# Optimization experiments

Hardware: AMD Instinct MI355X
Metric: run time of the kernel (lower is better)

## Reference

```python
import jax, jax.numpy as jnp
import numpy as np

B, N, M, D = 8, 1024, 2048, 1024


def setup_inputs() -> dict:
    key = jax.random.key(0)
    k1, k2, k3 = jax.random.split(key, 3)
    text_features = jax.random.normal(k1, (B, N, D), dtype=jnp.float32)
    audio_features = jax.random.normal(k2, (B, M, D), dtype=jnp.float32)
    sigma = jnp.ones((1,), dtype=jnp.float32)  # learnable bandwidth, initial_sigma=1.0
    # audio lengths in [M//4, M) so no softmax row is fully masked
    audio_lengths = jnp.maximum(
        jax.random.randint(k3, (B,), 0, M), M // 4
    ).astype(jnp.int32)
    return {
        "text_features": text_features,
        "audio_features": audio_features,
        "sigma": sigma,
        "audio_lengths": audio_lengths,
    }


def reference(text_features, audio_features, sigma, audio_lengths):
    b, n, d = text_features.shape
    m = audio_features.shape[1]
    s = jnp.abs(sigma[0]) + 1e-8

    # QK^T / sqrt(d)  -> (B, N, M)
    scores = jnp.einsum("bnd,bmd->bnm", text_features, audio_features) / jnp.sqrt(
        jnp.float32(d)
    )

    # Gaussian relative positional bias: -|i/N - j/M|^2 / (2 sigma^2)
    text_pos = jnp.arange(n, dtype=jnp.float32) / n    # (N,)
    audio_pos = jnp.arange(m, dtype=jnp.float32) / m   # (M,)
    d_rel = jnp.abs(text_pos[:, None] - audio_pos[None, :])  # (N, M)
    scores = scores - d_rel**2 / (2.0 * s * s)

    # mask padded audio positions per batch element
    valid = jnp.arange(m)[None, :] < audio_lengths[:, None]  # (B, M) bool
    scores = jnp.where(valid[:, None, :], scores, -jnp.inf)

    attention_weights = jax.nn.softmax(scores, axis=-1)  # (B, N, M)
    enhanced = jnp.einsum("bnm,bmd->bnd", attention_weights, audio_features)
    return enhanced, attention_weights
```

## Files before the change

### kernel.cpp

```cpp
#include <hip/hip_runtime.h>
#include <hip/hip_bf16.h>

#define BB 8
#define NN 1024
#define MM 2048
#define DD 1024

typedef __attribute__((ext_vector_type(8))) __bf16 bfrag8;
typedef __attribute__((ext_vector_type(4))) float ffrag4;

__device__ __forceinline__ unsigned short f2bf(float f) {
  union { float f; unsigned u; } x; x.f = f;
  unsigned r = x.u + 0x7FFFu + ((x.u >> 16) & 1u);
  return (unsigned short)(r >> 16);
}

__device__ __forceinline__ void gload_lds16(const unsigned short* g, unsigned short* l) {
  __builtin_amdgcn_global_load_lds(
      (const __attribute__((address_space(1))) void*)g,
      (__attribute__((address_space(3))) void*)l, 16, 0, 0);
}

#define SCHED0() __builtin_amdgcn_sched_barrier(0)
#define MFMA16x16x32 __builtin_amdgcn_mfma_f32_16x16x32_bf16

__device__ __forceinline__ void stage_half(const unsigned short* gbase, int ldk,
                                           unsigned short* ldst,
                                           int w, int r0, int slog) {
  const unsigned short* g = gbase + (size_t)(w * 8 + r0) * ldk + slog;
  gload_lds16(g, ldst + w * 512);
  gload_lds16(g + (size_t)64 * ldk, ldst + 4096 + w * 512);
}

__device__ __forceinline__ void stage_op32(const unsigned short* gbase, int ldk,
                                           unsigned short* L,
                                           int w, int srow, int sloc) {
  const unsigned short* g0 = gbase + (size_t)(w * 32 + srow) * ldk + sloc;
  gload_lds16(g0, L + w * 1024);
  gload_lds16(g0 + (size_t)16 * ldk, L + w * 1024 + 512);
}

#define TSTR 68
__global__ __launch_bounds__(256) void ta_prep(
    const float* __restrict__ Q, const float* __restrict__ V,
    unsigned short* __restrict__ Qbf,
    unsigned short* __restrict__ Kbf, unsigned short* __restrict__ VT,
    float* __restrict__ sums)
{
  __shared__ unsigned short Tls[64 * TSTR];
  const int bid = blockIdx.x;
  const int t = threadIdx.x;

  if (bid < 4096) {
    int tt = bid * 256 + t;
    const float4* src = reinterpret_cast<const float4*>(Q) + tt * 2;
    float4 a = src[0], b = src[1];
    ushort4 lo = { f2bf(a.x), f2bf(a.y), f2bf(a.z), f2bf(a.w) };
    ushort4 hi = { f2bf(b.x), f2bf(b.y), f2bf(b.z), f2bf(b.w) };
    ushort4* dst = reinterpret_cast<ushort4*>(Qbf) + tt * 2;
    dst[0] = lo; dst[1] = hi;
  } else if (bid < 8192) {
    const int id = bid - 4096;
    const int dt = id & 15;
    const int mt = (id >> 4) & 31;
    const int b  = id >> 9;

    const float* Vb = V + (size_t)b * MM * DD + (size_t)(mt * 64) * DD + dt * 64;
#pragma unroll
    for (int it = 0; it < 4; ++it) {
      int slot = t + 256 * it;
      int row  = slot >> 4;
      int c4   = slot & 15;
      float4 a = *reinterpret_cast<const float4*>(Vb + (size_t)row * DD + c4 * 4);
      ushort4 h = { f2bf(a.x), f2bf(a.y), f2bf(a.z), f2bf(a.w) };
      *reinterpret_cast<ushort4*>(&Tls[row * TSTR + c4 * 4]) = h;
    }
    __syncthreads();

    unsigned short* Kb = Kbf + (size_t)b * MM * DD + (size_t)(mt * 64) * DD + dt * 64;
    unsigned short* Vt = VT  + (size_t)b * DD * MM + (size_t)(dt * 64) * MM + mt * 64;
#pragma unroll
    for (int it = 0; it < 4; ++it) {
      int slot = t + 256 * it;
      int row  = slot >> 4;
      int c4   = slot & 15;
      *reinterpret_cast<ushort4*>(Kb + (size_t)row * DD + c4 * 4) =
          *reinterpret_cast<const ushort4*>(&Tls[row * TSTR + c4 * 4]);
      ushort4 tv = { Tls[(c4 * 4 + 0) * TSTR + row],
                     Tls[(c4 * 4 + 1) * TSTR + row],
                     Tls[(c4 * 4 + 2) * TSTR + row],
                     Tls[(c4 * 4 + 3) * TSTR + row] };
      *reinterpret_cast<ushort4*>(Vt + (size_t)row * MM + c4 * 4) = tv;
    }
  } else {
    int tt = (bid - 8192) * 256 + t;
    sums[tt] = 0.0f;
  }
}

__global__ void ta_zero(float* __restrict__ sums) {
  int t = blockIdx.x * 256 + threadIdx.x;
  if (t < BB * NN) sums[t] = 0.0f;
}

__global__ __launch_bounds__(512, 2) void ta_gemm1x(
    const unsigned short* __restrict__ Q,
    const unsigned short* __restrict__ K,
    const float* __restrict__ sigma,
    const int* __restrict__ lens,
    unsigned short* __restrict__ Ebf,
    float* __restrict__ rowsum)
{
  const int lin = blockIdx.x + 8 * (blockIdx.y + 4 * blockIdx.z);
  const int wid = (lin & 7) * 32 + (lin >> 3);
  const int bj = wid & 7, bi = (wid >> 3) & 3, b = wid >> 5;

  const int t = threadIdx.x;
  const int lane = t & 63, w = t >> 6;
  const int wr = w >> 2, wc = w & 3;
  __shared__ unsigned short S[73728];

  const unsigned short* Qb = Q + (size_t)b * NN * DD + (size_t)(bi * 256) * DD;
  const unsigned short* Kb = K + (size_t)b * MM * DD + (size_t)(bj * 256) * DD;

  const int r  = lane & 15, qd = lane >> 4;
  const int srow = lane >> 2;
  const int sloc = ((lane & 3) ^ (srow & 3)) << 3;
  const int fco  = (qd ^ (r & 3)) << 3;

  ffrag4 acc[8][4] = {};

  {
    stage_op32(Qb,      DD, &S[0],            w, srow, sloc);
    stage_op32(Kb,      DD, &S[8192],         w, srow, sloc);
    stage_op32(Qb + 32, DD, &S[16384],        w, srow, sloc);
    stage_op32(Kb + 32, DD, &S[16384 + 8192], w, srow, sloc);
    stage_op32(Qb + 64, DD, &S[32768],        w, srow, sloc);
    stage_op32(Kb + 64, DD, &S[32768 + 8192], w, srow, sloc);
    asm volatile("s_waitcnt vmcnt(8)" ::: "memory");
    __builtin_amdgcn_s_barrier();
  }

#pragma unroll 4
  for (int kt = 0; kt < 32; ++kt) {
    unsigned short* Buf = &S[(kt & 3) * 16384];

    if (kt + 3 < 32) {
      unsigned short* D = &S[((kt + 3) & 3) * 16384];
      const int k0 = (kt + 3) * 32;
      stage_op32(Qb + k0, DD, D,        w, srow, sloc);
      stage_op32(Kb + k0, DD, D + 8192, w, srow, sloc);
    }

    bfrag8 af[8], bf[4];
    const unsigned short* Ar = Buf + (wr * 128 + r) * 32 + fco;
    const unsigned short* Br = Buf + 8192 + (wc * 64 + r) * 32 + fco;
#pragma unroll
    for (int mi = 0; mi < 8; ++mi)
      af[mi] = *reinterpret_cast<const bfrag8*>(Ar + mi * 512);
#pragma unroll
    for (int nj = 0; nj < 4; ++nj)
      bf[nj] = *reinterpret_cast<const bfrag8*>(Br + nj * 512);

    asm volatile("s_waitcnt lgkmcnt(0)" ::: "memory");
    SCHED0(); __builtin_amdgcn_s_setprio(1);
#pragma unroll
    for (int mi = 0; mi < 8; ++mi)
#pragma unroll
      for (int nj = 0; nj < 4; ++nj)
        acc[mi][nj] = MFMA16x16x32(af[mi], bf[nj], acc[mi][nj], 0, 0, 0);
    __builtin_amdgcn_s_setprio(0); SCHED0();

    if (kt < 29)       { asm volatile("s_waitcnt vmcnt(8)" ::: "memory"); }
    else if (kt == 29) { asm volatile("s_waitcnt vmcnt(4)" ::: "memory"); }
    else if (kt == 30) { asm volatile("s_waitcnt vmcnt(0)" ::: "memory"); }
    if (kt < 31) __builtin_amdgcn_s_barrier();
  }
  __syncthreads();

  const float sg = fabsf(sigma[0]) + 1e-8f;
  const float inv2s2 = 1.0f / (2.0f * sg * sg);
  const int len = lens[b];
  unsigned short* Erow = Ebf + (size_t)b * NN * MM;
  float* sums = rowsum + (size_t)b * NN;
  const int ibase = bi * 256 + wr * 128;
  const int jbase = bj * 256 + wc * 64;
  unsigned short* W = &S[w * 9216];

#pragma unroll
  for (int mi = 0; mi < 8; ++mi) {
#pragma unroll
    for (int v = 0; v < 4; ++v) {
      int lrow = mi * 16 + qd * 4 + v;
      int i = ibase + lrow;
      float psum = 0.0f;
#pragma unroll
      for (int nj = 0; nj < 4; ++nj) {
        int j = jbase + nj * 16 + r;
        float e = 0.0f;
        if (j < len) {
          float dr = (float)i * (1.0f / (float)NN) - (float)j * (1.0f / (float)MM);
          float sc = acc[mi][nj][v] * 0.03125f - dr * dr * inv2s2;
          e = __expf(fminf(sc, 30.0f));
        }
        psum += e;
        W[lrow * 72 + nj * 16 + r] = f2bf(e);
      }
      psum += __shfl_xor(psum, 1);
      psum += __shfl_xor(psum, 2);
      psum += __shfl_xor(psum, 4);
      psum += __shfl_xor(psum, 8);
      if (r == 0) atomicAdd(&sums[i], psum);
    }
  }
  asm volatile("s_waitcnt lgkmcnt(0)" ::: "memory");
  const int rrow = lane >> 3, c8 = lane & 7;
#pragma unroll
  for (int pp = 0; pp < 16; ++pp) {
    int row = pp * 8 + rrow;
    uint4 val = *reinterpret_cast<const uint4*>(&W[row * 72 + c8 * 8]);
    *reinterpret_cast<uint4*>(Erow + (size_t)(ibase + row) * MM + jbase + c8 * 8) = val;
  }
}

__global__ __launch_bounds__(512, 2) void ta_gemm2x(
    const unsigned short* __restrict__ E,
    const unsigned short* __restrict__ VT,
    const float* __restrict__ rowsum,
    float* __restrict__ O,
    float* __restrict__ attn)
{
  const int lin = blockIdx.x + 4 * (blockIdx.y + 8 * blockIdx.z);
  const int wid = (lin & 7) * 32 + (lin >> 3);
  const int bd = wid & 3, bi = (wid >> 2) & 7, b = wid >> 5;

  const int t = threadIdx.x;
  const int lane = t & 63, w = t >> 6;
  const int wr = w >> 2, wc = w & 3;
  __shared__ unsigned short S[73728];

  const unsigned short* Eb = E  + (size_t)b * NN * MM + (size_t)(bi * 128) * MM;
  const unsigned short* Vb = VT + (size_t)b * DD * MM + (size_t)(bd * 256) * MM;

  const int r  = lane & 15, qd = lane >> 4;
  const int r0 = (lane >> 3) & 7;
  const int slog = ((lane & 7) ^ r0) << 3;
  const int cs0 = ((qd)     ^ (r & 7)) << 3;
  const int cs1 = ((4 + qd) ^ (r & 7)) << 3;

  ffrag4 acc[4][4] = {};

  const float* rsB = rowsum + (size_t)b * NN;
  const int arow = t >> 2;
  const int lcb  = (t & 3) * 2;
  const int apc0 = (lcb)     ^ (arow & 7);
  const int apc1 = (lcb + 1) ^ (arow & 7);
  const float ainv = 1.0f / fmaxf(rsB[bi * 128 + arow], 1e-30f);
  float* attnRowBase = attn + ((size_t)b * NN + bi * 128 + arow) * MM;

  {
    stage_half(Eb,                        MM, &S[0],     w, r0, slog);
    stage_half(Vb,                        MM, &S[8192],  w, r0, slog);
    stage_half(Vb + (size_t)128 * MM,     MM, &S[16384], w, r0, slog);
    stage_half(Eb + 64,                    MM, &S[24576],         w, r0, slog);
    stage_half(Vb + 64,                    MM, &S[24576 + 8192],  w, r0, slog);
    stage_half(Vb + (size_t)128 * MM + 64, MM, &S[24576 + 16384], w, r0, slog);
    asm volatile("s_waitcnt vmcnt(6)" ::: "memory");
    __builtin_amdgcn_s_barrier();
  }

  int cur = 0;
  for (int kt = 0; kt < 32; ++kt) {
    unsigned short* Tb = &S[cur * 24576];
    unsigned short* Ab = Tb;
    unsigned short* Bb = Tb + 8192 + (wc >> 1) * 8192;
    const int arb = wr * 64;
    const int brb = (wc & 1) * 64;

    if (kt + 2 < 32) {
      int nb = cur + 2; if (nb >= 3) nb -= 3;
      unsigned short* D = &S[nb * 24576];
      const int k0 = (kt + 2) * 64;
      stage_half(Eb + k0,                    MM, D,         w, r0, slog);
      stage_half(Vb + k0,                    MM, D + 8192,  w, r0, slog);
      stage_half(Vb + (size_t)128 * MM + k0, MM, D + 16384, w, r0, slog);
    }

    bfrag8 af[4][2], bf[4][2];
#pragma unroll
    for (int mi = 0; mi < 4; ++mi) {
      const unsigned short* a = &Ab[(arb + mi * 16 + r) * 64];
      af[mi][0] = *reinterpret_cast<const bfrag8*>(a + cs0);
      af[mi][1] = *reinterpret_cast<const bfrag8*>(a + cs1);
    }
#pragma unroll
    for (int nj = 0; nj < 4; ++nj) {
      const unsigned short* bp = &Bb[(brb + nj * 16 + r) * 64];
      bf[nj][0] = *reinterpret_cast<const bfrag8*>(bp + cs0);
      bf[nj][1] = *reinterpret_cast<const bfrag8*>(bp + cs1);
    }

    if ((kt >> 3) == bd) {
      uint4 av0 = *reinterpret_cast<const uint4*>(&Ab[arow * 64 + apc0 * 8]);
      uint4 av1 = *reinterpret_cast<const uint4*>(&Ab[arow * 64 + apc1 * 8]);
      float* dst = attnRowBase + kt * 64 + lcb * 8;
      unsigned u[8] = { av0.x, av0.y, av0.z, av0.w, av1.x, av1.y, av1.z, av1.w };
      float o[16];
#pragma unroll
      for (int k2 = 0; k2 < 8; ++k2) {
        union { unsigned u; float f; } lo, hi;
        lo.u = u[k2] << 16; hi.u = u[k2] & 0xFFFF0000u;
        o[2 * k2]     = lo.f * ainv;
        o[2 * k2 + 1] = hi.f * ainv;
      }
      float4* d4 = reinterpret_cast<float4*>(dst);
      float4 f0 = { o[0],  o[1],  o[2],  o[3]  };
      float4 f1 = { o[4],  o[5],  o[6],  o[7]  };
      float4 f2 = { o[8],  o[9],  o[10], o[11] };
      float4 f3 = { o[12], o[13], o[14], o[15] };
      d4[0] = f0; d4[1] = f1; d4[2] = f2; d4[3] = f3;
    }

    asm volatile("s_waitcnt lgkmcnt(0)" ::: "memory");
    SCHED0(); __builtin_amdgcn_s_setprio(1);
#pragma unroll
    for (int mi = 0; mi < 4; ++mi)
#pragma unroll
      for (int nj = 0; nj < 4; ++nj) {
        acc[mi][nj] = MFMA16x16x32(af[mi][0], bf[nj][0], acc[mi][nj], 0, 0, 0);
        acc[mi][nj] = MFMA16x16x32(af[mi][1], bf[nj][1], acc[mi][nj], 0, 0, 0);
      }
    __builtin_amdgcn_s_setprio(0); SCHED0();

    if (kt < 30)       { asm volatile("s_waitcnt vmcnt(6)" ::: "memory"); }
    else if (kt == 30) { asm volatile("s_waitcnt vmcnt(0)" ::: "memory"); }
    if (kt < 31) __builtin_amdgcn_s_barrier();
    cur += 1; if (cur == 3) cur = 0;
  }

  float* Ob = O + (size_t)b * NN * DD;
  const int ibase = bi * 128 + wr * 64;
  const int dbase = bd * 256 + wc * 64;
#pragma unroll
  for (int mi = 0; mi < 4; ++mi) {
#pragma unroll
    for (int v = 0; v < 4; ++v) {
      int i = ibase + mi * 16 + qd * 4 + v;
      float inv = 1.0f / fmaxf(rsB[i], 1e-30f);
#pragma unroll
      for (int nj = 0; nj < 4; ++nj) {
        int d = dbase + nj * 16 + r;
        Ob[(size_t)i * DD + d] = acc[mi][nj][v] * inv;
      }
    }
  }
}

#define LDA 40
__global__ __launch_bounds__(256) void tb_gemm1e(
    const float* __restrict__ Q, const float* __restrict__ K,
    const float* __restrict__ sigma, const int* __restrict__ lens,
    float* __restrict__ attn, float* __restrict__ rowsum)
{
  const int bj = blockIdx.x, bi = blockIdx.y, b = blockIdx.z;
  const int t = threadIdx.x;
  const int lane = t & 63;
  const int w = t >> 6;
  const int wi = w >> 1, wj = w & 1;
  __shared__ unsigned short Als[128 * LDA];
  __shared__ unsigned short Bls[128 * LDA];
  const float* Qb = Q + (size_t)b * NN * DD + (size_t)(bi * 128) * DD;
  const float* Kb = K + (size_t)b * MM * DD + (size_t)(bj * 128) * DD;
  ffrag4 acc[4][4] = {};
  const int r = lane & 15;
  const int koff = (lane >> 4) * 8;
  for (int k0 = 0; k0 < DD; k0 += 32) {
#pragma unroll
    for (int it = 0; it < 4; ++it) {
      int slot = t + 256 * it;
      int row = slot >> 3, c4 = slot & 7;
      float4 qa = *reinterpret_cast<const float4*>(Qb + (size_t)row * DD + k0 + c4 * 4);
      float4 ka = *reinterpret_cast<const float4*>(Kb + (size_t)row * DD + k0 + c4 * 4);
      ushort4 qh = { f2bf(qa.x), f2bf(qa.y), f2bf(qa.z), f2bf(qa.w) };
      ushort4 kh = { f2bf(ka.x), f2bf(ka.y), f2bf(ka.z), f2bf(ka.w) };
      *reinterpret_cast<ushort4*>(&Als[row * LDA + c4 * 4]) = qh;
      *reinterpret_cast<ushort4*>(&Bls[row * LDA + c4 * 4]) = kh;
    }
    __syncthreads();
    bfrag8 af[4], bf[4];
#pragma unroll
    for (int ti = 0; ti < 4; ++ti)
      af[ti] = *reinterpret_cast<const bfrag8*>(&Als[(wi * 64 + ti * 16 + r) * LDA + koff]);
#pragma unroll
    for (int tj = 0; tj < 4; ++tj)
      bf[tj] = *reinterpret_cast<const bfrag8*>(&Bls[(wj * 64 + tj * 16 + r) * LDA + koff]);
#pragma unroll
    for (int ti = 0; ti < 4; ++ti)
#pragma unroll
      for (int tj = 0; tj < 4; ++tj)
        acc[ti][tj] = MFMA16x16x32(af[ti], bf[tj], acc[ti][tj], 0, 0, 0);
    __syncthreads();
  }
  const float s = fabsf(sigma[0]) + 1e-8f;
  const float inv2s2 = 1.0f / (2.0f * s * s);
  const int len = lens[b];
  float* Prow = attn + (size_t)b * NN * MM;
  float* sums = rowsum + (size_t)b * NN;
  const int ibase = bi * 128 + wi * 64;
  const int jbase = bj * 128 + wj * 64;
  const int quad = lane >> 4;
#pragma unroll
  for (int ti = 0; ti < 4; ++ti) {
#pragma unroll
    for (int v = 0; v < 4; ++v) {
      int i = ibase + ti * 16 + quad * 4 + v;
      float psum = 0.0f;
#pragma unroll
      for (int tj = 0; tj < 4; ++tj) {
        int j = jbase + tj * 16 + r;
        float e = 0.0f;
        if (j < len) {
          float dr = (float)i * (1.0f / (float)NN) - (float)j * (1.0f / (float)MM);
          float sc = acc[ti][tj][v] * 0.03125f - dr * dr * inv2s2;
          e = __expf(fminf(sc, 30.0f));
        }
        psum += e;
        Prow[(size_t)i * MM + j] = e;
      }
      psum += __shfl_xor(psum, 1);
      psum += __shfl_xor(psum, 2);
      psum += __shfl_xor(psum, 4);
      psum += __shfl_xor(psum, 8);
      if (r == 0) atomicAdd(&sums[i], psum);
    }
  }
}

__global__ __launch_bounds__(256) void tb_norm(float* __restrict__ attn,
                                               const float* __restrict__ sums) {
  int t = blockIdx.x * 256 + threadIdx.x;
  int row = t >> 9;
  const float inv = 1.0f / fmaxf(sums[row], 1e-30f);
  float4* p = reinterpret_cast<float4*>(attn) + t;
  float4 x = *p;
  x.x *= inv; x.y *= inv; x.z *= inv; x.w *= inv;
  *p = x;
}

__global__ __launch_bounds__(256) void tb_gemm2(
    const float* __restrict__ P, const float* __restrict__ V, float* __restrict__ O)
{
  const int bd = blockIdx.x, bi = blockIdx.y, b = blockIdx.z;
  const int t = threadIdx.x;
  const int lane = t & 63;
  const int w = t >> 6;
  const int wi = w >> 1, wj = w & 1;
  __shared__ unsigned short Pls[128 * LDA];
  __shared__ unsigned short Vls[128 * LDA];
  const float* Pb = P + (size_t)b * NN * MM + (size_t)(bi * 128) * MM;
  const float* Vb = V + (size_t)b * MM * DD + bd * 128;
  ffrag4 acc[4][4] = {};
  const int r = lane & 15;
  const int koff = (lane >> 4) * 8;
  const int vd = t & 127;
  const int vmb = (t >> 7) * 16;
  for (int k0 = 0; k0 < MM; k0 += 32) {
#pragma unroll
    for (int it = 0; it < 4; ++it) {
      int slot = t + 256 * it;
      int row = slot >> 3, c4 = slot & 7;
      float4 pa = *reinterpret_cast<const float4*>(Pb + (size_t)row * MM + k0 + c4 * 4);
      ushort4 ph = { f2bf(pa.x), f2bf(pa.y), f2bf(pa.z), f2bf(pa.w) };
      *reinterpret_cast<ushort4*>(&Pls[row * LDA + c4 * 4]) = ph;
    }
    union { unsigned short h[16]; uint4 q[2]; } hv;
#pragma unroll
    for (int i = 0; i < 16; ++i)
      hv.h[i] = f2bf(Vb[(size_t)(k0 + vmb + i) * DD + vd]);
    *reinterpret_cast<uint4*>(&Vls[vd * LDA + vmb]) = hv.q[0];
    *reinterpret_cast<uint4*>(&Vls[vd * LDA + vmb + 8]) = hv.q[1];
    __syncthreads();
    bfrag8 af[4], bf[4];
#pragma unroll
    for (int ti = 0; ti < 4; ++ti)
      af[ti] = *reinterpret_cast<const bfrag8*>(&Pls[(wi * 64 + ti * 16 + r) * LDA + koff]);
#pragma unroll
    for (int tj = 0; tj < 4; ++tj)
      bf[tj] = *reinterpret_cast<const bfrag8*>(&Vls[(wj * 64 + tj * 16 + r) * LDA + koff]);
#pragma unroll
    for (int ti = 0; ti < 4; ++ti)
#pragma unroll
      for (int tj = 0; tj < 4; ++tj)
        acc[ti][tj] = MFMA16x16x32(af[ti], bf[tj], acc[ti][tj], 0, 0, 0);
    __syncthreads();
  }
  float* Ob = O + (size_t)b * NN * DD;
  const int ibase = bi * 128 + wi * 64;
  const int dbase = bd * 128 + wj * 64;
#pragma unroll
  for (int ti = 0; ti < 4; ++ti) {
#pragma unroll
    for (int tj = 0; tj < 4; ++tj) {
      int d = dbase + tj * 16 + r;
#pragma unroll
      for (int v = 0; v < 4; ++v) {
        int i = ibase + ti * 16 + (lane >> 4) * 4 + v;
        Ob[(size_t)i * DD + d] = acc[ti][tj][v];
      }
    }
  }
}

extern "C" void kernel_launch(void* const* d_in, const int* in_sizes, int n_in,
                              void* d_out, int out_size, void* d_ws, size_t ws_size,
                              hipStream_t stream) {
  const float* text  = (const float*)d_in[0];
  const float* audio = (const float*)d_in[1];
  const float* sigma = (const float*)d_in[2];
  const int*   lens  = (const int*)d_in[3];

  float* out = (float*)d_out;
  float* enhanced = out;
  float* attn = out + (size_t)BB * NN * DD;

  const size_t QBF  = (size_t)BB * NN * DD * 2;
  const size_t KBF  = (size_t)BB * MM * DD * 2;
  const size_t VTB  = (size_t)BB * DD * MM * 2;
  const size_t EBF  = (size_t)BB * NN * MM * 2;
  const size_t offQ = 65536;
  const size_t offK = offQ + QBF;
  const size_t offV = offK + KBF;
  const size_t offE = offV + VTB;
  const size_t need = offE + EBF;

  float* rowsum = (float*)d_ws;

  if (ws_size >= need) {
    unsigned short* Qbf = (unsigned short*)((char*)d_ws + offQ);
    unsigned short* Kbf = (unsigned short*)((char*)d_ws + offK);
    unsigned short* VT  = (unsigned short*)((char*)d_ws + offV);
    unsigned short* Ebf = (unsigned short*)((char*)d_ws + offE);

    ta_prep<<<dim3(8224), 256, 0, stream>>>(text, audio, Qbf, Kbf, VT, rowsum);
    ta_gemm1x<<<dim3(MM / 256, NN / 256, BB), 512, 0, stream>>>(Qbf, Kbf, sigma, lens, Ebf, rowsum);
    ta_gemm2x<<<dim3(DD / 256, NN / 128, BB), 512, 0, stream>>>(Ebf, VT, rowsum, enhanced, attn);
  } else {
    ta_zero<<<dim3((BB * NN + 255) / 256), 256, 0, stream>>>(rowsum);
    tb_gemm1e<<<dim3(MM / 128, NN / 128, BB), 256, 0, stream>>>(text, audio, sigma, lens, attn, rowsum);
    tb_norm<<<dim3(BB * NN * MM / 4 / 256), 256, 0, stream>>>(attn, rowsum);
    tb_gemm2<<<dim3(DD / 128, NN / 128, BB), 256, 0, stream>>>(attn, audio, enhanced);
  }
}
```

Before: 269.9 us.

## Shrink GEMM tiles to 128x128 with double-buffered LDS for higher occupancy

Both bf16 MFMA GEMM kernels move from 256-wide tiles with 3-4 stage LDS pipelines to 128x128 tiles with a two-stage K=64 buffer and a smaller LDS footprint. Launch bounds are raised so four blocks can share a CU. Each iteration now splits its MFMA work into two halves with the next stage's global-to-LDS loads issued between them. The first GEMM writes exp scores straight to global memory instead of staging them through LDS. The smaller tiles mean less operand reuse and more global traffic, and the direct stores are narrow and uncoalesced.

Measured after the change: 282.8 us. +4.7%, slower.

```diff
diff --git a/kernel.cpp b/kernel.cpp
--- a/kernel.cpp
+++ b/kernel.cpp
@@ -30,14 +30,6 @@
   const unsigned short* g = gbase + (size_t)(w * 8 + r0) * ldk + slog;
   gload_lds16(g, ldst + w * 512);
   gload_lds16(g + (size_t)64 * ldk, ldst + 4096 + w * 512);
-}
-
-__device__ __forceinline__ void stage_op32(const unsigned short* gbase, int ldk,
-                                           unsigned short* L,
-                                           int w, int srow, int sloc) {
-  const unsigned short* g0 = gbase + (size_t)(w * 32 + srow) * ldk + sloc;
-  gload_lds16(g0, L + w * 1024);
-  gload_lds16(g0 + (size_t)16 * ldk, L + w * 1024 + 512);
 }
 
 #define TSTR 68
@@ -103,7 +95,7 @@
   if (t < BB * NN) sums[t] = 0.0f;
 }
 
-__global__ __launch_bounds__(512, 2) void ta_gemm1x(
+__global__ __launch_bounds__(512, 4) void ta_gemm1x(
     const unsigned short* __restrict__ Q,
     const unsigned short* __restrict__ K,
     const float* __restrict__ sigma,
@@ -111,91 +103,101 @@
     unsigned short* __restrict__ Ebf,
     float* __restrict__ rowsum)
 {
-  const int lin = blockIdx.x + 8 * (blockIdx.y + 4 * blockIdx.z);
-  const int wid = (lin & 7) * 32 + (lin >> 3);
-  const int bj = wid & 7, bi = (wid >> 3) & 3, b = wid >> 5;
+  const int lin = blockIdx.x + 16 * (blockIdx.y + 8 * blockIdx.z);
+  const int wid = (lin & 7) * 128 + (lin >> 3);
+  const int bj = wid & 15, bi = (wid >> 4) & 7, b = wid >> 7;
 
   const int t = threadIdx.x;
   const int lane = t & 63, w = t >> 6;
   const int wr = w >> 2, wc = w & 3;
-  __shared__ unsigned short S[73728];
-
-  const unsigned short* Qb = Q + (size_t)b * NN * DD + (size_t)(bi * 256) * DD;
-  const unsigned short* Kb = K + (size_t)b * MM * DD + (size_t)(bj * 256) * DD;
+  __shared__ unsigned short S[32768];
+
+  const unsigned short* Qb = Q + (size_t)b * NN * DD + (size_t)(bi * 128) * DD;
+  const unsigned short* Kb = K + (size_t)b * MM * DD + (size_t)(bj * 128) * DD;
 
   const int r  = lane & 15, qd = lane >> 4;
-  const int srow = lane >> 2;
-  const int sloc = ((lane & 3) ^ (srow & 3)) << 3;
-  const int fco  = (qd ^ (r & 3)) << 3;
-
-  ffrag4 acc[8][4] = {};
+  const int r0 = (lane >> 3) & 7;
+  const int slog = ((lane & 7) ^ r0) << 3;
+  const int cs0 = ((qd)     ^ (r & 7)) << 3;
+  const int cs1 = ((4 + qd) ^ (r & 7)) << 3;
+
+  ffrag4 acc[4][2] = {};
 
   {
-    stage_op32(Qb,      DD, &S[0],            w, srow, sloc);
-    stage_op32(Kb,      DD, &S[8192],         w, srow, sloc);
-    stage_op32(Qb + 32, DD, &S[16384],        w, srow, sloc);
-    stage_op32(Kb + 32, DD, &S[16384 + 8192], w, srow, sloc);
-    stage_op32(Qb + 64, DD, &S[32768],        w, srow, sloc);
-    stage_op32(Kb + 64, DD, &S[32768 + 8192], w, srow, sloc);
-    asm volatile("s_waitcnt vmcnt(8)" ::: "memory");
+    stage_half(Qb,      DD, &S[0],             w, r0, slog);
+    stage_half(Kb,      DD, &S[8192],          w, r0, slog);
+    stage_half(Qb + 64, DD, &S[16384],         w, r0, slog);
+    stage_half(Kb + 64, DD, &S[16384 + 8192],  w, r0, slog);
+    asm volatile("s_waitcnt vmcnt(4)" ::: "memory");
     __builtin_amdgcn_s_barrier();
   }
 
-#pragma unroll 4
-  for (int kt = 0; kt < 32; ++kt) {
-    unsigned short* Buf = &S[(kt & 3) * 16384];
-
-    if (kt + 3 < 32) {
-      unsigned short* D = &S[((kt + 3) & 3) * 16384];
-      const int k0 = (kt + 3) * 32;
-      stage_op32(Qb + k0, DD, D,        w, srow, sloc);
-      stage_op32(Kb + k0, DD, D + 8192, w, srow, sloc);
-    }
-
-    bfrag8 af[8], bf[4];
-    const unsigned short* Ar = Buf + (wr * 128 + r) * 32 + fco;
-    const unsigned short* Br = Buf + 8192 + (wc * 64 + r) * 32 + fco;
-#pragma unroll
-    for (int mi = 0; mi < 8; ++mi)
-      af[mi] = *reinterpret_cast<const bfrag8*>(Ar + mi * 512);
-#pragma unroll
-    for (int nj = 0; nj < 4; ++nj)
-      bf[nj] = *reinterpret_cast<const bfrag8*>(Br + nj * 512);
+  for (int kt = 0; kt < 16; ++kt) {
+    unsigned short* Tb = &S[(kt & 1) * 16384];
+    bfrag8 af[4][2], bf[2][2];
+
+#pragma unroll
+    for (int mi = 0; mi < 4; ++mi) {
+      const unsigned short* a = &Tb[(wr * 64 + mi * 16 + r) * 64];
+      af[mi][0] = *reinterpret_cast<const bfrag8*>(a + cs0);
+      af[mi][1] = *reinterpret_cast<const bfrag8*>(a + cs1);
+    }
+#pragma unroll
+    for (int nj = 0; nj < 2; ++nj) {
+      const unsigned short* bp = &Tb[8192 + (wc * 32 + nj * 16 + r) * 64];
+      bf[nj][0] = *reinterpret_cast<const bfrag8*>(bp + cs0);
+      bf[nj][1] = *reinterpret_cast<const bfrag8*>(bp + cs1);
+    }
 
     asm volatile("s_waitcnt lgkmcnt(0)" ::: "memory");
+    SCHED0(); __builtin_amdgcn_s_barrier();
+
+    __builtin_amdgcn_s_setprio(1);
+#pragma unroll
+    for (int mi = 0; mi < 2; ++mi)
+#pragma unroll
+      for (int nj = 0; nj < 2; ++nj) {
+        acc[mi][nj] = MFMA16x16x32(af[mi][0], bf[nj][0], acc[mi][nj], 0, 0, 0);
+        acc[mi][nj] = MFMA16x16x32(af[mi][1], bf[nj][1], acc[mi][nj], 0, 0, 0);
+      }
+    __builtin_amdgcn_s_setprio(0); SCHED0();
+
+    if (kt + 2 < 16) {
+      const int k0 = (kt + 2) * 64;
+      stage_half(Qb + k0, DD, Tb,        w, r0, slog);
+      stage_half(Kb + k0, DD, Tb + 8192, w, r0, slog);
+    }
+
     SCHED0(); __builtin_amdgcn_s_setprio(1);
 #pragma unroll
-    for (int mi = 0; mi < 8; ++mi)
-#pragma unroll
-      for (int nj = 0; nj < 4; ++nj)
-        acc[mi][nj] = MFMA16x16x32(af[mi], bf[nj], acc[mi][nj], 0, 0, 0);
+    for (int mi = 2; mi < 4; ++mi)
+#pragma unroll
+      for (int nj = 0; nj < 2; ++nj) {
+        acc[mi][nj] = MFMA16x16x32(af[mi][0], bf[nj][0], acc[mi][nj], 0, 0, 0);
+        acc[mi][nj] = MFMA16x16x32(af[mi][1], bf[nj][1], acc[mi][nj], 0, 0, 0);
+      }
     __builtin_amdgcn_s_setprio(0); SCHED0();
 
-    if (kt < 29)       { asm volatile("s_waitcnt vmcnt(8)" ::: "memory"); }
-    else if (kt == 29) { asm volatile("s_waitcnt vmcnt(4)" ::: "memory"); }
-    else if (kt == 30) { asm volatile("s_waitcnt vmcnt(0)" ::: "memory"); }
-    if (kt < 31) __builtin_amdgcn_s_barrier();
-  }
-  __syncthreads();
+    if (kt < 14)       { asm volatile("s_waitcnt vmcnt(4)" ::: "memory"); }
+    else if (kt == 14) { asm volatile("s_waitcnt vmcnt(0)" ::: "memory"); }
+    if (kt < 15) __builtin_amdgcn_s_barrier();
+  }
 
   const float sg = fabsf(sigma[0]) + 1e-8f;
   const float inv2s2 = 1.0f / (2.0f * sg * sg);
   const int len = lens[b];
   unsigned short* Erow = Ebf + (size_t)b * NN * MM;
   float* sums = rowsum + (size_t)b * NN;
-  const int ibase = bi * 256 + wr * 128;
-  const int jbase = bj * 256 + wc * 64;
-  unsigned short* W = &S[w * 9216];
-
-#pragma unroll
-  for (int mi = 0; mi < 8; ++mi) {
+  const int ibase = bi * 128 + wr * 64;
+  const int jbase = bj * 128 + wc * 32;
+#pragma unroll
+  for (int mi = 0; mi < 4; ++mi) {
 #pragma unroll
     for (int v = 0; v < 4; ++v) {
-      int lrow = mi * 16 + qd * 4 + v;
-      int i = ibase + lrow;
+      int i = ibase + mi * 16 + qd * 4 + v;
       float psum = 0.0f;
 #pragma unroll
-      for (int nj = 0; nj < 4; ++nj) {
+      for (int nj = 0; nj < 2; ++nj) {
         int j = jbase + nj * 16 + r;
         float e = 0.0f;
         if (j < len) {
@@ -204,7 +206,7 @@
           e = __expf(fminf(sc, 30.0f));
         }
         psum += e;
-        W[lrow * 72 + nj * 16 + r] = f2bf(e);
+        Erow[(size_t)i * MM + j] = f2bf(e);
       }
       psum += __shfl_xor(psum, 1);
       psum += __shfl_xor(psum, 2);
@@ -213,34 +215,26 @@
       if (r == 0) atomicAdd(&sums[i], psum);
     }
   }
-  asm volatile("s_waitcnt lgkmcnt(0)" ::: "memory");
-  const int rrow = lane >> 3, c8 = lane & 7;
-#pragma unroll
-  for (int pp = 0; pp < 16; ++pp) {
-    int row = pp * 8 + rrow;
-    uint4 val = *reinterpret_cast<const uint4*>(&W[row * 72 + c8 * 8]);
-    *reinterpret_cast<uint4*>(Erow + (size_t)(ibase + row) * MM + jbase + c8 * 8) = val;
-  }
-}
-
-__global__ __launch_bounds__(512, 2) void ta_gemm2x(
+}
+
+__global__ __launch_bounds__(512, 4) void ta_gemm2x(
     const unsigned short* __restrict__ E,
     const unsigned short* __restrict__ VT,
     const float* __restrict__ rowsum,
     float* __restrict__ O,
     float* __restrict__ attn)
 {
-  const int lin = blockIdx.x + 4 * (blockIdx.y + 8 * blockIdx.z);
-  const int wid = (lin & 7) * 32 + (lin >> 3);
-  const int bd = wid & 3, bi = (wid >> 2) & 7, b = wid >> 5;
+  const int lin = blockIdx.x + 8 * (blockIdx.y + 8 * blockIdx.z);
+  const int wid = (lin & 7) * 64 + (lin >> 3);
+  const int bd = wid & 7, bi = (wid >> 3) & 7, b = wid >> 6;
 
   const int t = threadIdx.x;
   const int lane = t & 63, w = t >> 6;
   const int wr = w >> 2, wc = w & 3;
-  __shared__ unsigned short S[73728];
+  __shared__ unsigned short S[32768];
 
   const unsigned short* Eb = E  + (size_t)b * NN * MM + (size_t)(bi * 128) * MM;
-  const unsigned short* Vb = VT + (size_t)b * DD * MM + (size_t)(bd * 256) * MM;
+  const unsigned short* Vb = VT + (size_t)b * DD * MM + (size_t)(bd * 128) * MM;
 
   const int r  = lane & 15, qd = lane >> 4;
   const int r0 = (lane >> 3) & 7;
@@ -248,7 +242,7 @@
   const int cs0 = ((qd)     ^ (r & 7)) << 3;
   const int cs1 = ((4 + qd) ^ (r & 7)) << 3;
 
-  ffrag4 acc[4][4] = {};
+  ffrag4 acc[4][2] = {};
 
   const float* rsB = rowsum + (size_t)b * NN;
   const int arow = t >> 2;
@@ -259,50 +253,41 @@
   float* attnRowBase = attn + ((size_t)b * NN + bi * 128 + arow) * MM;
 
   {
-    stage_half(Eb,                        MM, &S[0],     w, r0, slog);
-    stage_half(Vb,                        MM, &S[8192],  w, r0, slog);
-    stage_half(Vb + (size_t)128 * MM,     MM, &S[16384], w, r0, slog);
-    stage_half(Eb + 64,                    MM, &S[24576],         w, r0, slog);
-    stage_half(Vb + 64,                    MM, &S[24576 + 8192],  w, r0, slog);
-    stage_half(Vb + (size_t)128 * MM + 64, MM, &S[24576 + 16384], w, r0, slog);
-    asm volatile("s_waitcnt vmcnt(6)" ::: "memory");
+    stage_half(Eb,      MM, &S[0],             w, r0, slog);
+    stage_half(Vb,      MM, &S[8192],          w, r0, slog);
+    stage_half(Eb + 64, MM, &S[16384],         w, r0, slog);
+    stage_half(Vb + 64, MM, &S[16384 + 8192],  w, r0, slog);
+    asm volatile("s_waitcnt vmcnt(4)" ::: "memory");
     __builtin_amdgcn_s_barrier();
   }
 
-  int cur = 0;
   for (int kt = 0; kt < 32; ++kt) {
-    unsigned short* Tb = &S[cur * 24576];
-    unsigned short* Ab = Tb;
-    unsigned short* Bb = Tb + 8192 + (wc >> 1) * 8192;
-    const int arb = wr * 64;
-    const int brb = (wc & 1) * 64;
-
-    if (kt + 2 < 32) {
-      int nb = cur + 2; if (nb >= 3) nb -= 3;
-      unsigned short* D = &S[nb * 24576];
-      const int k0 = (kt + 2) * 64;
-      stage_half(Eb + k0,                    MM, D,         w, r0, slog);
-      stage_half(Vb + k0,                    MM, D + 8192,  w, r0, slog);
-      stage_half(Vb + (size_t)128 * MM + k0, MM, D + 16384, w, r0, slog);
-    }
-
-    bfrag8 af[4][2], bf[4][2];
+    unsigned short* Tb = &S[(kt & 1) * 16384];
+    bfrag8 af[4][2], bf[2][2];
+    const bool awin = ((kt >> 2) == bd);
+    uint4 av0, av1;
+
 #pragma unroll
     for (int mi = 0; mi < 4; ++mi) {
-      const unsigned short* a = &Ab[(arb + mi * 16 + r) * 64];
+      const unsigned short* a = &Tb[(wr * 64 + mi * 16 + r) * 64];
       af[mi][0] = *reinterpret_cast<const bfrag8*>(a + cs0);
       af[mi][1] = *reinterpret_cast<const bfrag8*>(a + cs1);
     }
 #pragma unroll
-    for (int nj = 0; nj < 4; ++nj) {
-      const unsigned short* bp = &Bb[(brb + nj * 16 + r) * 64];
+    for (int nj = 0; nj < 2; ++nj) {
+      const unsigned short* bp = &Tb[8192 + (wc * 32 + nj * 16 + r) * 64];
       bf[nj][0] = *reinterpret_cast<const bfrag8*>(bp + cs0);
       bf[nj][1] = *reinterpret_cast<const bfrag8*>(bp + cs1);
     }
-
-    if ((kt >> 3) == bd) {
-      uint4 av0 = *reinterpret_cast<const uint4*>(&Ab[arow * 64 + apc0 * 8]);
-      uint4 av1 = *reinterpret_cast<const uint4*>(&Ab[arow * 64 + apc1 * 8]);
+    if (awin) {
+      av0 = *reinterpret_cast<const uint4*>(&Tb[arow * 64 + apc0 * 8]);
+      av1 = *reinterpret_cast<const uint4*>(&Tb[arow * 64 + apc1 * 8]);
+    }
+
+    asm volatile("s_waitcnt lgkmcnt(0)" ::: "memory");
+    SCHED0(); __builtin_amdgcn_s_barrier();
+
+    if (awin) {
       float* dst = attnRowBase + kt * 64 + lcb * 8;
       unsigned u[8] = { av0.x, av0.y, av0.z, av0.w, av1.x, av1.y, av1.z, av1.w };
       float o[16];
@@ -320,27 +305,42 @@
       float4 f3 = { o[12], o[13], o[14], o[15] };
       d4[0] = f0; d4[1] = f1; d4[2] = f2; d4[3] = f3;
     }
-
-    asm volatile("s_waitcnt lgkmcnt(0)" ::: "memory");
-    SCHED0(); __builtin_amdgcn_s_setprio(1);
-#pragma unroll
-    for (int mi = 0; mi < 4; ++mi)
-#pragma unroll
-      for (int nj = 0; nj < 4; ++nj) {
+    SCHED0();
+
+    __builtin_amdgcn_s_setprio(1);
+#pragma unroll
+    for (int mi = 0; mi < 2; ++mi)
+#pragma unroll
+      for (int nj = 0; nj < 2; ++nj) {
         acc[mi][nj] = MFMA16x16x32(af[mi][0], bf[nj][0], acc[mi][nj], 0, 0, 0);
         acc[mi][nj] = MFMA16x16x32(af[mi][1], bf[nj][1], acc[mi][nj], 0, 0, 0);
       }
     __builtin_amdgcn_s_setprio(0); SCHED0();
 
-    if (kt < 30)       { asm volatile("s_waitcnt vmcnt(6)" ::: "memory"); }
+    if (kt + 2 < 32) {
+      const int k0 = (kt + 2) * 64;
+      stage_half(Eb + k0, MM, Tb,        w, r0, slog);
+      stage_half(Vb + k0, MM, Tb + 8192, w, r0, slog);
+    }
+
+    SCHED0(); __builtin_amdgcn_s_setprio(1);
+#pragma unroll
+    for (int mi = 2; mi < 4; ++mi)
+#pragma unroll
+      for (int nj = 0; nj < 2; ++nj) {
+        acc[mi][nj] = MFMA16x16x32(af[mi][0], bf[nj][0], acc[mi][nj], 0, 0, 0);
+        acc[mi][nj] = MFMA16x16x32(af[mi][1], bf[nj][1], acc[mi][nj], 0, 0, 0);
+      }
+    __builtin_amdgcn_s_setprio(0); SCHED0();
+
+    if (kt < 30)       { asm volatile("s_waitcnt vmcnt(4)" ::: "memory"); }
     else if (kt == 30) { asm volatile("s_waitcnt vmcnt(0)" ::: "memory"); }
     if (kt < 31) __builtin_amdgcn_s_barrier();
-    cur += 1; if (cur == 3) cur = 0;
   }
 
   float* Ob = O + (size_t)b * NN * DD;
   const int ibase = bi * 128 + wr * 64;
-  const int dbase = bd * 256 + wc * 64;
+  const int dbase = bd * 128 + wc * 32;
 #pragma unroll
   for (int mi = 0; mi < 4; ++mi) {
 #pragma unroll
@@ -348,7 +348,7 @@
       int i = ibase + mi * 16 + qd * 4 + v;
       float inv = 1.0f / fmaxf(rsB[i], 1e-30f);
 #pragma unroll
-      for (int nj = 0; nj < 4; ++nj) {
+      for (int nj = 0; nj < 2; ++nj) {
         int d = dbase + nj * 16 + r;
         Ob[(size_t)i * DD + d] = acc[mi][nj][v] * inv;
       }
@@ -542,8 +542,8 @@
     unsigned short* Ebf = (unsigned short*)((char*)d_ws + offE);
 
     ta_prep<<<dim3(8224), 256, 0, stream>>>(text, audio, Qbf, Kbf, VT, rowsum);
-    ta_gemm1x<<<dim3(MM / 256, NN / 256, BB), 512, 0, stream>>>(Qbf, Kbf, sigma, lens, Ebf, rowsum);
-    ta_gemm2x<<<dim3(DD / 256, NN / 128, BB), 512, 0, stream>>>(Ebf, VT, rowsum, enhanced, attn);
+    ta_gemm1x<<<dim3(MM / 128, NN / 128, BB), 512, 0, stream>>>(Qbf, Kbf, sigma, lens, Ebf, rowsum);
+    ta_gemm2x<<<dim3(DD / 128, NN / 128, BB), 512, 0, stream>>>(Ebf, VT, rowsum, enhanced, attn);
   } else {
     ta_zero<<<dim3((BB * NN + 255) / 256), 256, 0, stream>>>(rowsum);
     tb_gemm1e<<<dim3(MM / 128, NN / 128, BB), 256, 0, stream>>>(text, audio, sigma, lens, attn, rowsum);
```
